# Performance work log

Hardware: AMD Instinct MI355X
Metric: run time of the kernel (lower is better)

The kernel has to match this reference:

```python
import jax, jax.numpy as jnp
import numpy as np

G = 128   # long_term_attn_g
H = 8     # num_attn_heads


def setup_inputs() -> dict:
    key = jax.random.key(0)
    ks = jax.random.split(key, 8)
    b, d, t, dk = 8, 1024, 8192, 512  # dk = model_dim // 2
    return {
        "qk": jax.random.normal(ks[0], (b, d, t), jnp.float32),
        "masks": jnp.ones((b, 1, t), jnp.float32),
        "wq": jax.random.normal(ks[1], (dk, d), jnp.float32) * 0.02,
        "bq": jnp.zeros((dk,), jnp.float32),
        "wk": jax.random.normal(ks[2], (dk, d), jnp.float32) * 0.02,
        "bk": jnp.zeros((dk,), jnp.float32),
        "wv": jax.random.normal(ks[3], (dk, d), jnp.float32) * 0.02,
        "bv": jnp.zeros((dk,), jnp.float32),
        "wo": jax.random.normal(ks[4], (d, dk), jnp.float32) * 0.02,
        "bo": jnp.zeros((d,), jnp.float32),
    }


def _to_patches(x, g):
    # convert_to_patches + rearrange 'b d np p -> (b p) d np'
    b, d, t = x.shape
    pad = (-t) % g
    x = jnp.pad(x, ((0, 0), (0, 0), (0, pad)))
    npat = x.shape[-1] // g
    return x.reshape(b, d, npat, g).transpose(0, 3, 1, 2).reshape(b * g, d, npat)


def reference(qk, masks, wq, bq, wk, bk, wv, bv, wo, bo):
    b, d, t = qk.shape
    xp = _to_patches(qk, G)     # [(b g), d, npat]  -- q, k, v source
    mp = _to_patches(masks, G)  # [(b g), 1, npat]  -- key-side attention mask

    # pointwise Conv1d projections == per-timestep matmuls
    q = jnp.einsum('od,bdt->bot', wq, xp) + bq[:, None]
    k = jnp.einsum('od,bdt->bot', wk, xp) + bk[:, None]
    v = jnp.einsum('od,bdt->bot', wv, xp) + bv[:, None]

    dk = wq.shape[0]
    dh = dk // H
    bg, _, npat = q.shape
    qh = q.reshape(bg, H, dh, npat)
    kh = k.reshape(bg, H, dh, npat)
    vh = v.reshape(bg, H, dh, npat)

    scores = jnp.einsum('bhdi,bhdj->bhij', qh, kh) / jnp.sqrt(jnp.float32(dh))
    scores = jnp.where(mp[:, :, None, :] > 0, scores, jnp.float32(-1e9))
    attn = jax.nn.softmax(scores, axis=-1)
    out = jnp.einsum('bhij,bhdj->bhdi', attn, vh).reshape(bg, dk, npat)

    # out_proj = GELU -> Conv1d(dk -> model_dim, k=1)
    out = jax.nn.gelu(out, approximate=False)
    out = jnp.einsum('od,bdt->bot', wo, out) + bo[:, None]

    # undo reshape: '(b g) d np -> b d (np g)', trim padding
    out = out.reshape(b, G, d, npat).transpose(0, 2, 3, 1).reshape(b, d, npat * G)[:, :, :t]
    return out * masks
```

## Files before the change

kernel.cpp:

```cpp
#include <hip/hip_runtime.h>
#include <hip/hip_bf16.h>
#include <cmath>

typedef __attribute__((ext_vector_type(4))) float f32x4;
typedef __attribute__((ext_vector_type(8))) short s16x8;

typedef __attribute__((address_space(1))) const void glb_void_t;
typedef __attribute__((address_space(3))) void lds_void_t;

#define MFMA(a, b, c) __builtin_amdgcn_mfma_f32_16x16x32_bf16(a, b, c, 0, 0, 0)
#define GLOAD_LDS(g, l) __builtin_amdgcn_global_load_lds((glb_void_t*)(g), (lds_void_t*)(l), 16, 0, 0)

__device__ __forceinline__ unsigned short bf(float x) {
  union { float f; unsigned u; } c; c.f = x;
  unsigned r = (c.u + 0x7fffu + ((c.u >> 16) & 1u)) >> 16;
  return (unsigned short)r;
}

__global__ void k_prep(const float* __restrict__ wq, const float* __restrict__ wk,
                       const float* __restrict__ wv, const float* __restrict__ bq,
                       const float* __restrict__ bk, const float* __restrict__ bv,
                       const float* __restrict__ wo,
                       __hip_bfloat16* __restrict__ wqkv, __hip_bfloat16* __restrict__ wob,
                       float* __restrict__ bqkv) {
  const int NW = 1536 * 1024, NO = 1024 * 512;
  for (int i = blockIdx.x * blockDim.x + threadIdx.x; i < NW + NO + 1536;
       i += gridDim.x * blockDim.x) {
    if (i < NW) {
      int r = i >> 10;
      float v = (r < 512) ? wq[i] : ((r < 1024) ? wk[i - 512 * 1024] : wv[i - 1024 * 1024]);
      ((unsigned short*)wqkv)[i] = bf(v);
    } else if (i < NW + NO) {
      int j = i - NW;
      ((unsigned short*)wob)[j] = bf(wo[j]);
    } else {
      int j = i - NW - NO;
      bqkv[j] = (j < 512) ? bq[j] : ((j < 1024) ? bk[j - 512] : bv[j - 1024]);
    }
  }
}

__global__ __launch_bounds__(256) void k_transpose(const float* __restrict__ qk,
                                                   __hip_bfloat16* __restrict__ qkT) {
  __shared__ float tile[64][65];
  const int b = blockIdx.z, t0 = blockIdx.x * 64, d0 = blockIdx.y * 64;
  const int tid = threadIdx.x;
  const int tq = tid & 15, dr = tid >> 4;
  const float* src = qk + ((size_t)b * 1024 + d0) * 8192 + t0;
#pragma unroll
  for (int i = 0; i < 4; i++) {
    int d = dr + i * 16;
    float4 v = *(const float4*)(src + (size_t)d * 8192 + tq * 4);
    tile[d][tq * 4 + 0] = v.x; tile[d][tq * 4 + 1] = v.y;
    tile[d][tq * 4 + 2] = v.z; tile[d][tq * 4 + 3] = v.w;
  }
  __syncthreads();
  const int d4 = (tid & 15) * 4, tr = tid >> 4;
  unsigned short* dst = (unsigned short*)qkT + ((size_t)b * 8192 + t0) * 1024 + d0;
#pragma unroll
  for (int i = 0; i < 4; i++) {
    int t = tr + i * 16;
    ushort4 o4;
    o4.x = bf(tile[d4 + 0][t]); o4.y = bf(tile[d4 + 1][t]);
    o4.z = bf(tile[d4 + 2][t]); o4.w = bf(tile[d4 + 3][t]);
    *(ushort4*)(dst + (size_t)t * 1024 + d4) = o4;
  }
}

__global__ __launch_bounds__(512) void k_qkv(const __hip_bfloat16* __restrict__ qkT,
                                             const __hip_bfloat16* __restrict__ wqkv,
                                             const float* __restrict__ bqkv,
                                             __hip_bfloat16* __restrict__ qkv) {
  __shared__ char smem[128 * 128 + 256 * 128];
  char* As = smem;
  char* Bs = smem + 16384;
  const int b = blockIdx.z, t0 = blockIdx.x * 128, o0 = blockIdx.y * 256;
  const int tid = threadIdx.x, l = tid & 63, w = tid >> 6;
  const int c = l & 15, g = l >> 4;
  const int wm = w >> 2, wn = w & 3;
  const int lrow = l >> 3, lcol = (l & 7) * 16;

  f32x4 acc[4][4];
#pragma unroll
  for (int i = 0; i < 4; i++)
#pragma unroll
    for (int j = 0; j < 4; j++) acc[i][j] = (f32x4){0.f, 0.f, 0.f, 0.f};

  const char* qbase = (const char*)(qkT + ((size_t)b * 8192 + t0) * 1024);
  const char* wbase = (const char*)(wqkv + (size_t)o0 * 1024);

  for (int ks = 0; ks < 16; ks++) {
    __syncthreads();
#pragma unroll
    for (int ii = 0; ii < 2; ii++) {
      int row = w * 16 + ii * 8 + lrow;
      int cb = lcol ^ ((row & 7) << 4);
      const char* gp = qbase + (size_t)row * 2048 + ks * 128 + cb;
      GLOAD_LDS(gp, As + (w * 16 + ii * 8) * 128);
    }
#pragma unroll
    for (int ii = 0; ii < 4; ii++) {
      int row = w * 32 + ii * 8 + lrow;
      int cb = lcol ^ ((row & 7) << 4);
      const char* gp = wbase + (size_t)row * 2048 + ks * 128 + cb;
      GLOAD_LDS(gp, Bs + (w * 32 + ii * 8) * 128);
    }
    __syncthreads();
#pragma unroll
    for (int kk = 0; kk < 2; kk++) {
      s16x8 av[4], bv[4];
#pragma unroll
      for (int mi = 0; mi < 4; mi++) {
        int row = wm * 64 + mi * 16 + c;
        int cb = (kk * 64 + g * 16) ^ ((row & 7) << 4);
        av[mi] = *(const s16x8*)(As + row * 128 + cb);
      }
#pragma unroll
      for (int ni = 0; ni < 4; ni++) {
        int row = wn * 64 + ni * 16 + c;
        int cb = (kk * 64 + g * 16) ^ ((row & 7) << 4);
        bv[ni] = *(const s16x8*)(Bs + row * 128 + cb);
      }
#pragma unroll
      for (int mi = 0; mi < 4; mi++)
#pragma unroll
        for (int ni = 0; ni < 4; ni++)
          acc[mi][ni] = MFMA(av[mi], bv[ni], acc[mi][ni]);
    }
  }
  unsigned short* outb = (unsigned short*)qkv + ((size_t)b * 8192 + t0) * 1536 + o0;
  float bias[4];
#pragma unroll
  for (int ni = 0; ni < 4; ni++) bias[ni] = bqkv[o0 + wn * 64 + ni * 16 + c];
#pragma unroll
  for (int mi = 0; mi < 4; mi++)
#pragma unroll
    for (int r = 0; r < 4; r++) {
      int t = wm * 64 + mi * 16 + g * 4 + r;
#pragma unroll
      for (int ni = 0; ni < 4; ni++) {
        int o = wn * 64 + ni * 16 + c;
        outb[(size_t)t * 1536 + o] = bf(acc[mi][ni][r] + bias[ni]);
      }
    }
}

__global__ __launch_bounds__(64) void k_attn(const __hip_bfloat16* __restrict__ qkv,
                                             const float* __restrict__ masks,
                                             __hip_bfloat16* __restrict__ a_out) {
  const int l = threadIdx.x, c = l & 15, g = l >> 4;
  const int h = blockIdx.x & 7, bg = blockIdx.x >> 3;
  const int gg = bg & 127, b = bg >> 7;
  const size_t rowstep = (size_t)128 * 1536;
  const __hip_bfloat16* base = qkv + ((size_t)b * 8192 + gg) * 1536 + h * 64;
  const __hip_bfloat16* Qb = base;
  const __hip_bfloat16* Kb = base + 512;
  const __hip_bfloat16* Vb = base + 1024;

  s16x8 kf[4][2], qf[4][2];
#pragma unroll
  for (int f = 0; f < 4; f++)
#pragma unroll
    for (int kk = 0; kk < 2; kk++) {
      size_t roff = (size_t)(f * 16 + c) * rowstep + kk * 32 + g * 8;
      kf[f][kk] = *(const s16x8*)(Kb + roff);
      qf[f][kk] = *(const s16x8*)(Qb + roff);
    }
  f32x4 st[4][4];
#pragma unroll
  for (int i = 0; i < 4; i++)
#pragma unroll
    for (int j = 0; j < 4; j++) st[i][j] = (f32x4){0.f, 0.f, 0.f, 0.f};
#pragma unroll
  for (int mj = 0; mj < 4; mj++)
#pragma unroll
    for (int ni = 0; ni < 4; ni++)
#pragma unroll
      for (int kk = 0; kk < 2; kk++)
        st[mj][ni] = MFMA(kf[mj][kk], qf[ni][kk], st[mj][ni]);

  float mk[4][4];
#pragma unroll
  for (int mj = 0; mj < 4; mj++)
#pragma unroll
    for (int r = 0; r < 4; r++)
      mk[mj][r] = masks[(size_t)b * 8192 + (size_t)(mj * 16 + g * 4 + r) * 128 + gg];

  float inv[4];
#pragma unroll
  for (int ni = 0; ni < 4; ni++) {
    float m = -1e30f;
#pragma unroll
    for (int mj = 0; mj < 4; mj++)
#pragma unroll
      for (int r = 0; r < 4; r++) {
        float s = st[mj][ni][r] * 0.125f;
        s = (mk[mj][r] > 0.f) ? s : -1e9f;
        st[mj][ni][r] = s;
        m = fmaxf(m, s);
      }
    m = fmaxf(m, __shfl_xor(m, 16));
    m = fmaxf(m, __shfl_xor(m, 32));
    float sm = 0.f;
#pragma unroll
    for (int mj = 0; mj < 4; mj++)
#pragma unroll
      for (int r = 0; r < 4; r++) {
        float p = expf(st[mj][ni][r] - m);
        st[mj][ni][r] = p;
        sm += p;
      }
    sm += __shfl_xor(sm, 16);
    sm += __shfl_xor(sm, 32);
    inv[ni] = 1.f / sm;
  }
#pragma unroll
  for (int mj = 0; mj < 4; mj++)
#pragma unroll
    for (int ni = 0; ni < 4; ni++)
#pragma unroll
      for (int r = 0; r < 4; r++) st[mj][ni][r] *= inv[ni];

  unsigned qd[4][4][2];
#pragma unroll
  for (int ni = 0; ni < 4; ni++)
#pragma unroll
    for (int mj = 0; mj < 4; mj++)
#pragma unroll
      for (int wv = 0; wv < 2; wv++)
        qd[ni][mj][wv] = (unsigned)bf(st[mj][ni][2 * wv]) |
                         ((unsigned)bf(st[mj][ni][2 * wv + 1]) << 16);

  f32x4 oacc[4][4];
#pragma unroll
  for (int i = 0; i < 4; i++)
#pragma unroll
    for (int j = 0; j < 4; j++) oacc[i][j] = (f32x4){0.f, 0.f, 0.f, 0.f};

  const int srcA = c + 32 * (g & 1);
  const int srcB = srcA + 16;
  const bool hi = (g >= 2);
#pragma unroll
  for (int kk = 0; kk < 2; kk++) {
    s16x8 af[4];
#pragma unroll
    for (int ni = 0; ni < 4; ni++) {
      unsigned a0 = __shfl(qd[ni][2 * kk][0], srcA);
      unsigned b0 = __shfl(qd[ni][2 * kk + 1][0], srcA);
      unsigned a1 = __shfl(qd[ni][2 * kk][1], srcA);
      unsigned b1 = __shfl(qd[ni][2 * kk + 1][1], srcA);
      unsigned a2 = __shfl(qd[ni][2 * kk][0], srcB);
      unsigned b2 = __shfl(qd[ni][2 * kk + 1][0], srcB);
      unsigned a3 = __shfl(qd[ni][2 * kk][1], srcB);
      unsigned b3 = __shfl(qd[ni][2 * kk + 1][1], srcB);
      union { unsigned u[4]; s16x8 v; } uu;
      uu.u[0] = hi ? b0 : a0;
      uu.u[1] = hi ? b1 : a1;
      uu.u[2] = hi ? b2 : a2;
      uu.u[3] = hi ? b3 : a3;
      af[ni] = uu.v;
    }
    s16x8 bvv[4];
#pragma unroll
    for (int fd = 0; fd < 4; fd++) {
      s16x8 t;
#pragma unroll
      for (int e = 0; e < 8; e++)
        t[e] = *(const short*)(Vb + (size_t)(kk * 32 + g * 8 + e) * rowstep + fd * 16 + c);
      bvv[fd] = t;
    }
#pragma unroll
    for (int fi = 0; fi < 4; fi++)
#pragma unroll
      for (int fd = 0; fd < 4; fd++)
        oacc[fi][fd] = MFMA(af[fi], bvv[fd], oacc[fi][fd]);
  }

  unsigned short* ob = (unsigned short*)a_out + ((size_t)b * 8192 + gg) * 512 + h * 64;
#pragma unroll
  for (int fi = 0; fi < 4; fi++)
#pragma unroll
    for (int fd = 0; fd < 4; fd++)
#pragma unroll
      for (int r = 0; r < 4; r++) {
        float x = oacc[fi][fd][r];
        float ge = 0.5f * x * (1.f + erff(x * 0.70710678118f));
        int i = fi * 16 + g * 4 + r;
        ob[(size_t)i * (128 * 512) + fd * 16 + c] = bf(ge);
      }
}

__global__ __launch_bounds__(512) void k_out(const __hip_bfloat16* __restrict__ wob,
                                             const __hip_bfloat16* __restrict__ a,
                                             const float* __restrict__ bo,
                                             const float* __restrict__ masks,
                                             float* __restrict__ y) {
  __shared__ char smem[256 * 128 + 128 * 128];
  char* As = smem;
  char* Bs = smem + 32768;
  const int b = blockIdx.z, t0 = blockIdx.x * 128, o0 = blockIdx.y * 256;
  const int tid = threadIdx.x, l = tid & 63, w = tid >> 6;
  const int c = l & 15, g = l >> 4;
  const int wm = w >> 1, wn = w & 1;
  const int lrow = l >> 3, lcol = (l & 7) * 16;

  f32x4 acc[4][4];
#pragma unroll
  for (int i = 0; i < 4; i++)
#pragma unroll
    for (int j = 0; j < 4; j++) acc[i][j] = (f32x4){0.f, 0.f, 0.f, 0.f};

  const char* wbase = (const char*)(wob + (size_t)o0 * 512);
  const char* abase = (const char*)(a + ((size_t)b * 8192 + t0) * 512);

  for (int ks = 0; ks < 8; ks++) {
    __syncthreads();
#pragma unroll
    for (int ii = 0; ii < 4; ii++) {
      int row = w * 32 + ii * 8 + lrow;
      int cb = lcol ^ ((row & 7) << 4);
      const char* gp = wbase + (size_t)row * 1024 + ks * 128 + cb;
      GLOAD_LDS(gp, As + (w * 32 + ii * 8) * 128);
    }
#pragma unroll
    for (int ii = 0; ii < 2; ii++) {
      int row = w * 16 + ii * 8 + lrow;
      int cb = lcol ^ ((row & 7) << 4);
      const char* gp = abase + (size_t)row * 1024 + ks * 128 + cb;
      GLOAD_LDS(gp, Bs + (w * 16 + ii * 8) * 128);
    }
    __syncthreads();
#pragma unroll
    for (int kk = 0; kk < 2; kk++) {
      s16x8 av[4], bv[4];
#pragma unroll
      for (int mi = 0; mi < 4; mi++) {
        int row = wm * 64 + mi * 16 + c;
        int cb = (kk * 64 + g * 16) ^ ((row & 7) << 4);
        av[mi] = *(const s16x8*)(As + row * 128 + cb);
      }
#pragma unroll
      for (int ni = 0; ni < 4; ni++) {
        int row = wn * 64 + ni * 16 + c;
        int cb = (kk * 64 + g * 16) ^ ((row & 7) << 4);
        bv[ni] = *(const s16x8*)(Bs + row * 128 + cb);
      }
#pragma unroll
      for (int mi = 0; mi < 4; mi++)
#pragma unroll
        for (int ni = 0; ni < 4; ni++)
          acc[mi][ni] = MFMA(av[mi], bv[ni], acc[mi][ni]);
    }
  }
  int tcol[4];
  float mk[4];
#pragma unroll
  for (int ni = 0; ni < 4; ni++) {
    tcol[ni] = t0 + wn * 64 + ni * 16 + c;
    mk[ni] = masks[(size_t)b * 8192 + tcol[ni]];
  }
#pragma unroll
  for (int mi = 0; mi < 4; mi++)
#pragma unroll
    for (int r = 0; r < 4; r++) {
      int od = o0 + wm * 64 + mi * 16 + g * 4 + r;
      float bias = bo[od];
      float* yrow = y + ((size_t)b * 1024 + od) * 8192;
#pragma unroll
      for (int ni = 0; ni < 4; ni++)
        yrow[tcol[ni]] = (acc[mi][ni][r] + bias) * mk[ni];
    }
}

extern "C" void kernel_launch(void* const* d_in, const int* in_sizes, int n_in,
                              void* d_out, int out_size, void* d_ws, size_t ws_size,
                              hipStream_t stream) {
  const float* qk = (const float*)d_in[0];
  const float* masks = (const float*)d_in[1];
  const float* wq = (const float*)d_in[2];
  const float* bq = (const float*)d_in[3];
  const float* wk = (const float*)d_in[4];
  const float* bk = (const float*)d_in[5];
  const float* wv = (const float*)d_in[6];
  const float* bv = (const float*)d_in[7];
  const float* wo = (const float*)d_in[8];
  const float* bo = (const float*)d_in[9];

  char* ws = (char*)d_ws;
  __hip_bfloat16* qkT = (__hip_bfloat16*)ws;
  __hip_bfloat16* a = (__hip_bfloat16*)ws;
  __hip_bfloat16* wqkv = (__hip_bfloat16*)(ws + 134217728);
  __hip_bfloat16* wob = (__hip_bfloat16*)(ws + 134217728 + 3145728);
  float* bqkv = (float*)(ws + 134217728 + 3145728 + 1048576);

  __hip_bfloat16* qkv = (__hip_bfloat16*)d_out;
  float* y = (float*)d_out;

  k_prep<<<dim3(512), dim3(256), 0, stream>>>(wq, wk, wv, bq, bk, bv, wo, wqkv, wob, bqkv);
  k_transpose<<<dim3(128, 16, 8), dim3(256), 0, stream>>>(qk, qkT);
  k_qkv<<<dim3(64, 6, 8), dim3(512), 0, stream>>>(qkT, wqkv, bqkv, qkv);
  k_attn<<<dim3(8192), dim3(64), 0, stream>>>(qkv, masks, a);
  k_out<<<dim3(64, 4, 8), dim3(512), 0, stream>>>(wob, a, bo, masks, y);
}
```

Measured before the change: 477.4 us.

## Rewrite QKV GEMM with 256x256 tiles, double-buffered LDS, and interleaved prefetch

The QKV projection GEMM moves from 128x256 tiles to 256x256 tiles per 512-thread block. The K loop is rewritten as a double-buffered, HipKittens-style ping-pong schedule: global-to-LDS loads for the next tiles are issued between quadrant MFMA phases, with explicit vmcnt and lgkmcnt waits, barriers and setprio. This aims to hide global-load latency and cut weight re-reads, at the cost of 128KB of LDS, more accumulators per thread, and fewer blocks in the grid.

```diff
diff --git a/kernel.cpp b/kernel.cpp
--- a/kernel.cpp
+++ b/kernel.cpp
@@ -67,76 +67,145 @@
   }
 }
 
-__global__ __launch_bounds__(512) void k_qkv(const __hip_bfloat16* __restrict__ qkT,
-                                             const __hip_bfloat16* __restrict__ wqkv,
-                                             const float* __restrict__ bqkv,
-                                             __hip_bfloat16* __restrict__ qkv) {
-  __shared__ char smem[128 * 128 + 256 * 128];
-  char* As = smem;
-  char* Bs = smem + 16384;
-  const int b = blockIdx.z, t0 = blockIdx.x * 128, o0 = blockIdx.y * 256;
+__device__ __forceinline__ void stage_half(char* lds_base, const char* gbase,
+                                           int ktile, int w, int l) {
+#pragma unroll
+  for (int r = 0; r < 2; ++r) {
+    int row = r * 64 + w * 8 + (l >> 3);
+    int cb = ((l & 7) * 16) ^ ((row & 7) << 4);
+    GLOAD_LDS(gbase + (size_t)row * 2048 + (size_t)ktile * 128 + cb,
+              lds_base + (r * 64 + w * 8) * 128);
+  }
+}
+
+__global__ __launch_bounds__(512, 2) void k_qkv(const __hip_bfloat16* __restrict__ qkT,
+                                                const __hip_bfloat16* __restrict__ wqkv,
+                                                const float* __restrict__ bqkv,
+                                                __hip_bfloat16* __restrict__ qkv) {
+  __shared__ char smem[131072];
+  const int NT = 16;
+  const int b = blockIdx.z, t0 = blockIdx.x * 256, o0 = blockIdx.y * 256;
   const int tid = threadIdx.x, l = tid & 63, w = tid >> 6;
   const int c = l & 15, g = l >> 4;
   const int wm = w >> 2, wn = w & 3;
-  const int lrow = l >> 3, lcol = (l & 7) * 16;
-
-  f32x4 acc[4][4];
-#pragma unroll
-  for (int i = 0; i < 4; i++)
+  const int cbase = (g * 16) ^ ((c & 7) << 4);
+
+  const char* qpanel = (const char*)qkT + ((size_t)b * 8192 + t0) * 2048;
+  const char* wpanel = (const char*)wqkv + (size_t)o0 * 2048;
+
+#define STAGE_A(tt, h) stage_half(smem + ((tt)&1) * 32768 + (h) * 16384, \
+                                  qpanel + (size_t)(h) * 262144, (tt), w, l)
+#define STAGE_B(tt, h) stage_half(smem + 65536 + ((tt)&1) * 32768 + (h) * 16384, \
+                                  wpanel + (size_t)(h) * 262144, (tt), w, l)
+
+  f32x4 acc[8][4];
+#pragma unroll
+  for (int i = 0; i < 8; i++)
 #pragma unroll
     for (int j = 0; j < 4; j++) acc[i][j] = (f32x4){0.f, 0.f, 0.f, 0.f};
 
-  const char* qbase = (const char*)(qkT + ((size_t)b * 8192 + t0) * 1024);
-  const char* wbase = (const char*)(wqkv + (size_t)o0 * 1024);
-
-  for (int ks = 0; ks < 16; ks++) {
-    __syncthreads();
-#pragma unroll
-    for (int ii = 0; ii < 2; ii++) {
-      int row = w * 16 + ii * 8 + lrow;
-      int cb = lcol ^ ((row & 7) << 4);
-      const char* gp = qbase + (size_t)row * 2048 + ks * 128 + cb;
-      GLOAD_LDS(gp, As + (w * 16 + ii * 8) * 128);
-    }
-#pragma unroll
-    for (int ii = 0; ii < 4; ii++) {
-      int row = w * 32 + ii * 8 + lrow;
-      int cb = lcol ^ ((row & 7) << 4);
-      const char* gp = wbase + (size_t)row * 2048 + ks * 128 + cb;
-      GLOAD_LDS(gp, Bs + (w * 32 + ii * 8) * 128);
-    }
-    __syncthreads();
-#pragma unroll
-    for (int kk = 0; kk < 2; kk++) {
-      s16x8 av[4], bv[4];
-#pragma unroll
-      for (int mi = 0; mi < 4; mi++) {
-        int row = wm * 64 + mi * 16 + c;
-        int cb = (kk * 64 + g * 16) ^ ((row & 7) << 4);
-        av[mi] = *(const s16x8*)(As + row * 128 + cb);
-      }
-#pragma unroll
-      for (int ni = 0; ni < 4; ni++) {
-        int row = wn * 64 + ni * 16 + c;
-        int cb = (kk * 64 + g * 16) ^ ((row & 7) << 4);
-        bv[ni] = *(const s16x8*)(Bs + row * 128 + cb);
-      }
-#pragma unroll
-      for (int mi = 0; mi < 4; mi++)
-#pragma unroll
-        for (int ni = 0; ni < 4; ni++)
-          acc[mi][ni] = MFMA(av[mi], bv[ni], acc[mi][ni]);
-    }
-  }
+  STAGE_A(0, 0); STAGE_A(0, 1); STAGE_B(0, 0); STAGE_B(0, 1);
+  STAGE_B(1, 0); STAGE_A(1, 0); STAGE_A(1, 1);
+  asm volatile("s_waitcnt vmcnt(6)" ::: "memory");
+  __builtin_amdgcn_s_barrier();
+
+#pragma unroll 2
+  for (int t = 0; t < NT; ++t) {
+    const int buf = t & 1;
+    const char* Ah = smem + buf * 32768 + wm * 16384;
+    const char* Bh = smem + 65536 + buf * 32768 + (wn >> 1) * 16384;
+    const int brow = (wn & 1) * 64;
+    s16x8 avLo[4][2], avHi[4][2], bv[4][2];
+
+#pragma unroll
+    for (int mi = 0; mi < 4; ++mi)
+#pragma unroll
+      for (int kk = 0; kk < 2; ++kk)
+        avLo[mi][kk] = *(const s16x8*)(Ah + (mi * 16 + c) * 128 + (cbase ^ (kk << 6)));
+#pragma unroll
+    for (int ni = 0; ni < 4; ++ni)
+#pragma unroll
+      for (int kk = 0; kk < 2; ++kk)
+        bv[ni][kk] = *(const s16x8*)(Bh + (brow + ni * 16 + c) * 128 + (cbase ^ (kk << 6)));
+    if (t + 1 < NT) STAGE_B(t + 1, 1);
+    __builtin_amdgcn_s_barrier();
+    asm volatile("s_waitcnt lgkmcnt(0)" ::: "memory");
+    __builtin_amdgcn_sched_barrier(0);
+    __builtin_amdgcn_s_setprio(1);
+#pragma unroll
+    for (int mi = 0; mi < 4; ++mi)
+#pragma unroll
+      for (int ni = 0; ni < 2; ++ni)
+#pragma unroll
+        for (int kk = 0; kk < 2; ++kk)
+          acc[mi][ni] = MFMA(avLo[mi][kk], bv[ni][kk], acc[mi][ni]);
+    __builtin_amdgcn_s_setprio(0);
+    __builtin_amdgcn_s_barrier();
+
+#pragma unroll
+    for (int mi = 0; mi < 4; ++mi)
+#pragma unroll
+      for (int kk = 0; kk < 2; ++kk)
+        avHi[mi][kk] = *(const s16x8*)(Ah + (64 + mi * 16 + c) * 128 + (cbase ^ (kk << 6)));
+    if (t + 2 < NT) STAGE_B(t + 2, 0);
+    __builtin_amdgcn_s_barrier();
+    asm volatile("s_waitcnt lgkmcnt(0)" ::: "memory");
+    __builtin_amdgcn_sched_barrier(0);
+    __builtin_amdgcn_s_setprio(1);
+#pragma unroll
+    for (int mi = 0; mi < 4; ++mi)
+#pragma unroll
+      for (int ni = 0; ni < 2; ++ni)
+#pragma unroll
+        for (int kk = 0; kk < 2; ++kk)
+          acc[mi][ni + 2] = MFMA(avLo[mi][kk], bv[ni + 2][kk], acc[mi][ni + 2]);
+    __builtin_amdgcn_s_setprio(0);
+    __builtin_amdgcn_s_barrier();
+
+    if (t + 2 < NT) STAGE_A(t + 2, 0);
+    __builtin_amdgcn_s_barrier();
+    __builtin_amdgcn_s_setprio(1);
+#pragma unroll
+    for (int mi = 0; mi < 4; ++mi)
+#pragma unroll
+      for (int ni = 0; ni < 2; ++ni)
+#pragma unroll
+        for (int kk = 0; kk < 2; ++kk)
+          acc[mi + 4][ni] = MFMA(avHi[mi][kk], bv[ni][kk], acc[mi + 4][ni]);
+    __builtin_amdgcn_s_setprio(0);
+    __builtin_amdgcn_s_barrier();
+
+    if (t + 2 < NT) STAGE_A(t + 2, 1);
+    if (t + 2 < NT) {
+      asm volatile("s_waitcnt vmcnt(6)" ::: "memory");
+    } else {
+      asm volatile("s_waitcnt vmcnt(0)" ::: "memory");
+    }
+    __builtin_amdgcn_s_barrier();
+    __builtin_amdgcn_sched_barrier(0);
+    __builtin_amdgcn_s_setprio(1);
+#pragma unroll
+    for (int mi = 0; mi < 4; ++mi)
+#pragma unroll
+      for (int ni = 0; ni < 2; ++ni)
+#pragma unroll
+        for (int kk = 0; kk < 2; ++kk)
+          acc[mi + 4][ni + 2] = MFMA(avHi[mi][kk], bv[ni + 2][kk], acc[mi + 4][ni + 2]);
+    __builtin_amdgcn_s_setprio(0);
+    __builtin_amdgcn_s_barrier();
+  }
+#undef STAGE_A
+#undef STAGE_B
+
   unsigned short* outb = (unsigned short*)qkv + ((size_t)b * 8192 + t0) * 1536 + o0;
   float bias[4];
 #pragma unroll
   for (int ni = 0; ni < 4; ni++) bias[ni] = bqkv[o0 + wn * 64 + ni * 16 + c];
 #pragma unroll
-  for (int mi = 0; mi < 4; mi++)
+  for (int mi = 0; mi < 8; mi++)
 #pragma unroll
     for (int r = 0; r < 4; r++) {
-      int t = wm * 64 + mi * 16 + g * 4 + r;
+      int t = wm * 128 + mi * 16 + g * 4 + r;
 #pragma unroll
       for (int ni = 0; ni < 4; ni++) {
         int o = wn * 64 + ni * 16 + c;
@@ -398,7 +467,7 @@
 
   k_prep<<<dim3(512), dim3(256), 0, stream>>>(wq, wk, wv, bq, bk, bv, wo, wqkv, wob, bqkv);
   k_transpose<<<dim3(128, 16, 8), dim3(256), 0, stream>>>(qk, qkT);
-  k_qkv<<<dim3(64, 6, 8), dim3(512), 0, stream>>>(qkT, wqkv, bqkv, qkv);
+  k_qkv<<<dim3(32, 6, 8), dim3(512), 0, stream>>>(qkT, wqkv, bqkv, qkv);
   k_attn<<<dim3(8192), dim3(64), 0, stream>>>(qkv, masks, a);
   k_out<<<dim3(64, 4, 8), dim3(512), 0, stream>>>(wob, a, bo, masks, y);
 }
```

New measurement: 470.6 us. About the same (-1.4%).
